# Kernel optimization log

Measured on AMD Instinct MI355X. Metric: run time of the kernel, lower is better.

## Reference

```python
import jax, jax.numpy as jnp
import numpy as np

NUM_EDGES = 4000
NODES_PER_EDGE = 25
D_IN = 128
NUM_PROJ = 128
NUM_ANCHORS = 64
EPS = 1e-5


def sparse_sort(src, index):
    """Per-column stable sort of src (N,P), grouped by 1D segment index (N,).
    Mirrors the repo's sparse_sort: min-max normalize to [0,1] then add segment id."""
    fmin = src.min(axis=0, keepdims=True)
    fmax = src.max(axis=0, keepdims=True)
    norm = (src - fmin) / (fmax - fmin + 1e-12) + index[:, None].astype(src.dtype)
    perm = jnp.argsort(norm, axis=0, stable=True)  # (N, P)
    return jnp.take_along_axis(src, perm, axis=0), perm


def setup_inputs() -> dict:
    key = jax.random.key(0)
    k1, k2, k3 = jax.random.split(key, 3)
    n_inc = NUM_EDGES * NODES_PER_EDGE
    X = jax.random.normal(k1, (n_inc, D_IN), dtype=jnp.float32)
    # sorted segment ids, every edge has >=2 members -> double_self_loops is a no-op
    hyperedge_index = jnp.repeat(jnp.arange(NUM_EDGES, dtype=jnp.int32), NODES_PER_EDGE)
    theta_v = jax.random.normal(k2, (NUM_PROJ, D_IN), dtype=jnp.float32)
    # reference anchors: linspace(-1,1,M) replicated over projections (as in __init__)
    ref_anchors = jnp.tile(jnp.linspace(-1.0, 1.0, NUM_ANCHORS, dtype=jnp.float32)[:, None], (1, NUM_PROJ))
    weight = jax.random.normal(k3, (NUM_PROJ, NUM_ANCHORS), dtype=jnp.float32) * 0.1
    return {"X": X, "theta_v": theta_v, "ref_anchors": ref_anchors, "weight": weight,
            "hyperedge_index": hyperedge_index, "num_edges": NUM_EDGES}


def reference(X, theta_v, ref_anchors, weight, hyperedge_index, num_edges):
    P = theta_v.shape[0]
    M = ref_anchors.shape[0]
    dt = X.dtype
    # weight_norm with g=1: rows of v normalized to unit L2
    W = theta_v / jnp.linalg.norm(theta_v, axis=1, keepdims=True)
    Xslices = X @ W.T  # (N, P) slices
    Xslices_sorted, perm = sparse_sort(Xslices, hyperedge_index)
    seg = hyperedge_index[perm[:, 0]]  # segment id per sorted row (N,)
    N = seg.shape[0]
    # per-segment degree, pointer offsets
    D1 = jax.ops.segment_sum(jnp.ones(N, dt), seg, num_segments=num_edges)  # (E,)
    ptr = jnp.concatenate([jnp.zeros(1, dt), jnp.cumsum(D1)])
    D = D1[seg]
    Pofs = ptr[seg]
    R = jnp.arange(N, dtype=dt) + 1.0
    # sample positions: within-segment quantile in (0,1) + segment offset -> globally sorted
    x = (R - Pofs - 1.0) / (D - 1.0) * 0.99999 + EPS + seg.astype(dt)  # (N,)
    edges = jnp.arange(num_edges, dtype=jnp.int32)
    grid = jnp.linspace(0.0, 1.0, M).astype(dt) * 0.99998 + EPS  # (M,)
    xnew = (edges[:, None].astype(dt) + grid[None, :]).reshape(-1)  # (E*M,)
    # interp1d: x/xnew identical across projections -> one searchsorted, broadcast interp
    y = Xslices_sorted.T  # (P, N)
    ind = jnp.clip(jnp.searchsorted(x, xnew), 1, N - 1)  # (E*M,)
    x0, x1 = x[ind - 1], x[ind]
    t = ((xnew - x0) / (x1 - x0))[None, :]  # (1, E*M)
    ynew = y[:, ind - 1] + (y[:, ind] - y[:, ind - 1]) * t  # (P, E*M)
    Xsi = ynew.T  # (E*M, P)
    # reference slices per edge, sorted within segments (identity for sorted anchors)
    seg_anchor = jnp.repeat(edges, M)  # (E*M,)
    Rslices = jnp.tile(ref_anchors, (num_edges, 1))  # (E*M, P)
    _, Rind = sparse_sort(Rslices, seg_anchor)
    emb = Rslices - jnp.take_along_axis(Xsi, Rind, axis=0)  # (E*M, P)
    emb = emb.T.reshape(P, num_edges, M)
    out = (weight[:, None, :] * emb).mean(-1).T  # (E, P)
    return out, edges
```

## Files before the change

kernel.cpp:

```cpp
#include <hip/hip_runtime.h>
#include <math.h>

#define NEDGE 4000
#define NPE   25
#define DIN   128
#define NPROJ 128
#define NANCH 64
#define NROWS (NEDGE*NPE)
#define NBLK  (NROWS/32)

__device__ __forceinline__ float xval_of(int g) {
  int ee = g / NPE;
  int jj = g - ee * NPE;
  float t1 = __fdiv_rn((float)jj, 24.0f);
  float t2 = __fmul_rn(t1, 0.99999f);
  float t3 = __fadd_rn(t2, 1e-5f);
  return __fadd_rn(t3, (float)ee);
}

__global__ __launch_bounds__(128) void k_prep(const float* __restrict__ theta,
                                              const float* __restrict__ anchors,
                                              const float* __restrict__ weight,
                                              float* __restrict__ Wt,
                                              float* __restrict__ awT) {
  int p = threadIdx.x;
  float s = 0.f;
  #pragma unroll 8
  for (int k = 0; k < DIN; ++k) { float t = theta[p*DIN + k]; s = fmaf(t, t, s); }
  float nrm = sqrtf(s);
  for (int k = 0; k < DIN; ++k)
    Wt[k*NPROJ + p] = __fdiv_rn(theta[p*DIN + k], nrm);
  #pragma unroll
  for (int m = 0; m < NANCH; ++m) {
    awT[(2*m    )*NPROJ + p] = anchors[m*NPROJ + p];
    awT[(2*m + 1)*NPROJ + p] = weight[p*NANCH + m];
  }
}

__global__ __launch_bounds__(256) void k_gemm(const float* __restrict__ X,
                                              const float* __restrict__ Wt,
                                              float* __restrict__ Xs,
                                              float* __restrict__ pmin,
                                              float* __restrict__ pmax) {
  __shared__ float sW[32 * NPROJ];
  __shared__ float sX[32 * DIN];
  const int tid = threadIdx.x;
  const int rbase = blockIdx.x * 32;
  {
    const float4* src = (const float4*)(X + (size_t)rbase * DIN);
    float4* dst = (float4*)sX;
    #pragma unroll
    for (int i = 0; i < 4; ++i) dst[tid + 256*i] = src[tid + 256*i];
  }
  const int cg = tid & 31, rg = tid >> 5;
  const int p0 = cg * 4, r0 = rg * 4;
  float acc[4][4] = {};
  for (int ph = 0; ph < 4; ++ph) {
    __syncthreads();
    {
      const float4* src = (const float4*)(Wt + ph * 32 * NPROJ);
      float4* dst = (float4*)sW;
      #pragma unroll
      for (int i = 0; i < 4; ++i) dst[tid + 256*i] = src[tid + 256*i];
    }
    __syncthreads();
    #pragma unroll
    for (int k0 = 0; k0 < 32; k0 += 4) {
      float4 w[4];
      #pragma unroll
      for (int i = 0; i < 4; ++i) w[i] = *(const float4*)&sW[(k0+i)*NPROJ + p0];
      #pragma unroll
      for (int i = 0; i < 4; ++i) {
        float4 xv = *(const float4*)&sX[(r0+i)*DIN + ph*32 + k0];
        const float xs[4] = {xv.x, xv.y, xv.z, xv.w};
        #pragma unroll
        for (int kk = 0; kk < 4; ++kk) {
          acc[i][0] = fmaf(xs[kk], w[kk].x, acc[i][0]);
          acc[i][1] = fmaf(xs[kk], w[kk].y, acc[i][1]);
          acc[i][2] = fmaf(xs[kk], w[kk].z, acc[i][2]);
          acc[i][3] = fmaf(xs[kk], w[kk].w, acc[i][3]);
        }
      }
    }
  }
  #pragma unroll
  for (int i = 0; i < 4; ++i) {
    float4 st = make_float4(acc[i][0], acc[i][1], acc[i][2], acc[i][3]);
    *(float4*)&Xs[(size_t)(rbase + r0 + i)*NPROJ + p0] = st;
  }
  __syncthreads();
  float* rmn = sX;
  float* rmx = sX + 8*NPROJ;
  #pragma unroll
  for (int c = 0; c < 4; ++c) {
    float mn = fminf(fminf(acc[0][c], acc[1][c]), fminf(acc[2][c], acc[3][c]));
    float mx = fmaxf(fmaxf(acc[0][c], acc[1][c]), fmaxf(acc[2][c], acc[3][c]));
    rmn[rg*NPROJ + p0 + c] = mn;
    rmx[rg*NPROJ + p0 + c] = mx;
  }
  __syncthreads();
  if (tid < NPROJ) {
    float mn = rmn[tid], mx = rmx[tid];
    #pragma unroll
    for (int g2 = 1; g2 < 8; ++g2) {
      mn = fminf(mn, rmn[g2*NPROJ + tid]);
      mx = fmaxf(mx, rmx[g2*NPROJ + tid]);
    }
    pmin[(size_t)blockIdx.x*NPROJ + tid] = mn;
    pmax[(size_t)blockIdx.x*NPROJ + tid] = mx;
  }
}

__global__ __launch_bounds__(256) void k_red1(const float* __restrict__ pmin,
                                              const float* __restrict__ pmax,
                                              float* __restrict__ imn,
                                              float* __restrict__ imx) {
  __shared__ float smn[NPROJ], smx[NPROJ];
  const int tid = threadIdx.x, p = tid & 127, h = tid >> 7;
  const int b = blockIdx.x;
  float mn = INFINITY, mx = -INFINITY;
  for (int s = 125*b + h; s < 125*(b+1); s += 2) {
    mn = fminf(mn, pmin[(size_t)s*NPROJ + p]);
    mx = fmaxf(mx, pmax[(size_t)s*NPROJ + p]);
  }
  if (h == 1) { smn[p] = mn; smx[p] = mx; }
  __syncthreads();
  if (h == 0) {
    imn[b*NPROJ + p] = fminf(mn, smn[p]);
    imx[b*NPROJ + p] = fmaxf(mx, smx[p]);
  }
}

__global__ __launch_bounds__(256) void k_red2(const float* __restrict__ imn,
                                              const float* __restrict__ imx,
                                              float* __restrict__ fmn,
                                              float* __restrict__ fmx) {
  __shared__ float smn[NPROJ], smx[NPROJ];
  const int tid = threadIdx.x, p = tid & 127, h = tid >> 7;
  float mn = INFINITY, mx = -INFINITY;
  for (int s = h; s < 25; s += 2) {
    mn = fminf(mn, imn[s*NPROJ + p]);
    mx = fmaxf(mx, imx[s*NPROJ + p]);
  }
  if (h == 1) { smn[p] = mn; smx[p] = mx; }
  __syncthreads();
  if (h == 0) { fmn[p] = fminf(mn, smn[p]); fmx[p] = fmaxf(mx, smx[p]); }
}

__global__ __launch_bounds__(128) void k_sort(float* Xs,
                                              const float* __restrict__ fmnA,
                                              const float* __restrict__ fmxA) {
  __shared__ float svals[NPE * NPROJ];
  const int e = blockIdx.x;
  const int p = threadIdx.x;
  const float ef = (float)e;
  const float fmin = fmnA[p];
  const float denom = __fadd_rn(__fsub_rn(fmxA[p], fmin), 1e-12f);

  float v[NPE];
  unsigned ku[NPE];
  #pragma unroll
  for (int j = 0; j < NPE; ++j) {
    float x = Xs[(size_t)(e*NPE + j)*NPROJ + p];
    v[j] = x;
    ku[j] = __float_as_uint(__fadd_rn(__fdiv_rn(__fsub_rn(x, fmin), denom), ef));
  }
  #pragma unroll
  for (int i = 0; i < NPE; ++i) {
    int cnt = 0;
    #pragma unroll
    for (int j = 0; j < NPE; ++j) {
      if (j == i) continue;
      cnt += (j < i) ? (ku[j] <= ku[i]) : (ku[j] < ku[i]);
    }
    svals[cnt*NPROJ + p] = v[i];
  }
  #pragma unroll
  for (int j = 0; j < NPE; ++j)
    Xs[(size_t)(e*NPE + j)*NPROJ + p] = svals[j*NPROJ + p];
}

__global__ __launch_bounds__(128) void k_epi(const float* __restrict__ Xs,
                                             const float* __restrict__ awT,
                                             float* __restrict__ out) {
  __shared__ float sv[(NPE + 2) * NPROJ];
  __shared__ int   sind[NANCH];
  __shared__ float stt[NANCH];
  const int e = blockIdx.x;
  const int p = threadIdx.x;
  const float ef = (float)e;

  if (e > 0) {
    sv[p]         = Xs[(size_t)((e-1)*NPE + 23)*NPROJ + p];
    sv[NPROJ + p] = Xs[(size_t)((e-1)*NPE + 24)*NPROJ + p];
  }
  #pragma unroll
  for (int j = 0; j < NPE; ++j)
    sv[(2 + j)*NPROJ + p] = Xs[(size_t)(e*NPE + j)*NPROJ + p];

  if (p < NANCH) {
    const int m = p;
    const float delta = __fdiv_rn(1.0f, 63.0f);
    float g = __fmul_rn((float)m, delta);
    g = __fadd_rn(__fmul_rn(g, 0.99998f), 1e-5f);
    const float xnew = __fadd_rn(ef, g);
    int lo = e*NPE - 1; if (lo < 0) lo = 0;
    const int hi = e*NPE + (NPE - 1);
    int ind = -1;
    for (int j = lo; j <= hi; ++j) {
      float xg = xval_of(j);
      if (ind < 0 && xg >= xnew) ind = j;
    }
    if (ind < 0) ind = hi;
    if (ind < 1) ind = 1;
    float x0 = xval_of(ind - 1);
    float x1 = xval_of(ind);
    stt[m]  = __fdiv_rn(__fsub_rn(xnew, x0), __fsub_rn(x1, x0));
    sind[m] = ind;
  }
  __syncthreads();

  float acc = 0.f;
  const int base = e * NPE;
  for (int m = 0; m < NANCH; ++m) {
    const int ind = sind[m];
    const float t = stt[m];
    const int o1 = ind - base;
    const float y1 = sv[(o1 + 2)*NPROJ + p];
    const float y0 = sv[(o1 + 1)*NPROJ + p];
    const float ynew = __fadd_rn(y0, __fmul_rn(__fsub_rn(y1, y0), t));
    const float emb  = __fsub_rn(awT[(2*m)*NPROJ + p], ynew);
    acc = __fadd_rn(acc, __fmul_rn(awT[(2*m + 1)*NPROJ + p], emb));
  }
  out[(size_t)e*NPROJ + p] = __fmul_rn(acc, 0.015625f);
  if (p == 0) out[NEDGE*NPROJ + e] = (float)e;
}

extern "C" void kernel_launch(void* const* d_in, const int* in_sizes, int n_in,
                              void* d_out, int out_size, void* d_ws, size_t ws_size,
                              hipStream_t stream) {
  (void)in_sizes; (void)n_in; (void)out_size; (void)ws_size;
  const float* X      = (const float*)d_in[0];
  const float* theta  = (const float*)d_in[1];
  const float* anchor = (const float*)d_in[2];
  const float* weight = (const float*)d_in[3];
  float* out = (float*)d_out;
  float* ws  = (float*)d_ws;

  float* Xs   = ws;
  float* Wt   = Xs   + (size_t)NROWS*NPROJ;
  float* awT  = Wt   + DIN*NPROJ;
  float* pmin = awT  + 2*NANCH*NPROJ;
  float* pmax = pmin + (size_t)NBLK*NPROJ;
  float* imn  = pmax + (size_t)NBLK*NPROJ;
  float* imx  = imn  + 25*NPROJ;
  float* fmn  = imx  + 25*NPROJ;
  float* fmx  = fmn  + NPROJ;

  k_prep<<<1, 128, 0, stream>>>(theta, anchor, weight, Wt, awT);
  k_gemm<<<NBLK, 256, 0, stream>>>(X, Wt, Xs, pmin, pmax);
  k_red1<<<25, 256, 0, stream>>>(pmin, pmax, imn, imx);
  k_red2<<<1, 256, 0, stream>>>(imn, imx, fmn, fmx);
  k_sort<<<NEDGE, 128, 0, stream>>>(Xs, fmn, fmx);
  k_epi <<<NEDGE, 128, 0, stream>>>(Xs, awT, out);
}
```

Before: 219.3 us.

## Fuse per-edge sort into epilogue kernel and parallelize prep kernel

The separate sort kernel, which wrote the sorted slices back to global memory, is merged into the epilogue kernel. Each edge now sorts its 25 rows straight into shared memory. The two boundary values needed from the previous edge are recomputed by scanning that edge's 25 rows for its two largest keys, so no global write-back or re-read is needed. The prep kernel also goes from one 128-thread block with serial loops to 192 blocks. The cost is that every block reads its predecessor edge's data again and adds a selection pass.

```diff
diff --git a/kernel.cpp b/kernel.cpp
--- a/kernel.cpp
+++ b/kernel.cpp
@@ -23,17 +23,23 @@
                                               const float* __restrict__ weight,
                                               float* __restrict__ Wt,
                                               float* __restrict__ awT) {
-  int p = threadIdx.x;
-  float s = 0.f;
-  #pragma unroll 8
-  for (int k = 0; k < DIN; ++k) { float t = theta[p*DIN + k]; s = fmaf(t, t, s); }
-  float nrm = sqrtf(s);
-  for (int k = 0; k < DIN; ++k)
-    Wt[k*NPROJ + p] = __fdiv_rn(theta[p*DIN + k], nrm);
-  #pragma unroll
-  for (int m = 0; m < NANCH; ++m) {
-    awT[(2*m    )*NPROJ + p] = anchors[m*NPROJ + p];
-    awT[(2*m + 1)*NPROJ + p] = weight[p*NANCH + m];
+  __shared__ float snrm;
+  const int t = threadIdx.x;
+  if (blockIdx.x < NPROJ) {
+    const int p = blockIdx.x;
+    if (t == 0) {
+      float s = 0.f;
+      #pragma unroll 8
+      for (int k = 0; k < DIN; ++k) { float x = theta[p*DIN + k]; s = fmaf(x, x, s); }
+      snrm = sqrtf(s);
+    }
+    __syncthreads();
+    const float nrm = snrm;
+    Wt[t*NPROJ + p] = __fdiv_rn(theta[p*DIN + t], nrm);
+  } else {
+    const int m = blockIdx.x - NPROJ;
+    awT[(2*m    )*NPROJ + t] = anchors[m*NPROJ + t];
+    awT[(2*m + 1)*NPROJ + t] = weight[t*NANCH + m];
   }
 }
 
@@ -147,56 +153,57 @@
   if (h == 0) { fmn[p] = fminf(mn, smn[p]); fmx[p] = fmaxf(mx, smx[p]); }
 }
 
-__global__ __launch_bounds__(128) void k_sort(float* Xs,
+__global__ __launch_bounds__(128) void k_main(const float* __restrict__ Xs,
                                               const float* __restrict__ fmnA,
-                                              const float* __restrict__ fmxA) {
-  __shared__ float svals[NPE * NPROJ];
-  const int e = blockIdx.x;
-  const int p = threadIdx.x;
-  const float ef = (float)e;
-  const float fmin = fmnA[p];
-  const float denom = __fadd_rn(__fsub_rn(fmxA[p], fmin), 1e-12f);
-
-  float v[NPE];
-  unsigned ku[NPE];
-  #pragma unroll
-  for (int j = 0; j < NPE; ++j) {
-    float x = Xs[(size_t)(e*NPE + j)*NPROJ + p];
-    v[j] = x;
-    ku[j] = __float_as_uint(__fadd_rn(__fdiv_rn(__fsub_rn(x, fmin), denom), ef));
-  }
-  #pragma unroll
-  for (int i = 0; i < NPE; ++i) {
-    int cnt = 0;
-    #pragma unroll
-    for (int j = 0; j < NPE; ++j) {
-      if (j == i) continue;
-      cnt += (j < i) ? (ku[j] <= ku[i]) : (ku[j] < ku[i]);
-    }
-    svals[cnt*NPROJ + p] = v[i];
-  }
-  #pragma unroll
-  for (int j = 0; j < NPE; ++j)
-    Xs[(size_t)(e*NPE + j)*NPROJ + p] = svals[j*NPROJ + p];
-}
-
-__global__ __launch_bounds__(128) void k_epi(const float* __restrict__ Xs,
-                                             const float* __restrict__ awT,
-                                             float* __restrict__ out) {
+                                              const float* __restrict__ fmxA,
+                                              const float* __restrict__ awT,
+                                              float* __restrict__ out) {
   __shared__ float sv[(NPE + 2) * NPROJ];
   __shared__ int   sind[NANCH];
   __shared__ float stt[NANCH];
   const int e = blockIdx.x;
   const int p = threadIdx.x;
   const float ef = (float)e;
-
+  const float fmin = fmnA[p];
+  const float denom = __fadd_rn(__fsub_rn(fmxA[p], fmin), 1e-12f);
+
+  float v[NPE], pv[NPE];
+  #pragma unroll
+  for (int j = 0; j < NPE; ++j) v[j] = Xs[(size_t)(e*NPE + j)*NPROJ + p];
   if (e > 0) {
-    sv[p]         = Xs[(size_t)((e-1)*NPE + 23)*NPROJ + p];
-    sv[NPROJ + p] = Xs[(size_t)((e-1)*NPE + 24)*NPROJ + p];
-  }
+    #pragma unroll
+    for (int j = 0; j < NPE; ++j) pv[j] = Xs[(size_t)((e-1)*NPE + j)*NPROJ + p];
+  }
+
+  unsigned ku[NPE];
   #pragma unroll
   for (int j = 0; j < NPE; ++j)
-    sv[(2 + j)*NPROJ + p] = Xs[(size_t)(e*NPE + j)*NPROJ + p];
+    ku[j] = __float_as_uint(__fadd_rn(__fdiv_rn(__fsub_rn(v[j], fmin), denom), ef));
+  #pragma unroll
+  for (int i = 0; i < NPE; ++i) {
+    int cnt = 0;
+    #pragma unroll
+    for (int j = 0; j < NPE; ++j) {
+      if (j == i) continue;
+      cnt += (j < i) ? (ku[j] <= ku[i]) : (ku[j] < ku[i]);
+    }
+    sv[(2 + cnt)*NPROJ + p] = v[i];
+  }
+
+  if (e > 0) {
+    const float efp = (float)(e - 1);
+    unsigned k1 = 0u, k2 = 0u;
+    float v1 = 0.f, v2 = 0.f;
+    #pragma unroll
+    for (int j = 0; j < NPE; ++j) {
+      unsigned kk = __float_as_uint(
+          __fadd_rn(__fdiv_rn(__fsub_rn(pv[j], fmin), denom), efp));
+      if (kk >= k1)      { k2 = k1; v2 = v1; k1 = kk; v1 = pv[j]; }
+      else if (kk >= k2) { k2 = kk; v2 = pv[j]; }
+    }
+    sv[p]         = v2;
+    sv[NPROJ + p] = v1;
+  }
 
   if (p < NANCH) {
     const int m = p;
@@ -257,10 +264,9 @@
   float* fmn  = imx  + 25*NPROJ;
   float* fmx  = fmn  + NPROJ;
 
-  k_prep<<<1, 128, 0, stream>>>(theta, anchor, weight, Wt, awT);
+  k_prep<<<NPROJ + NANCH, 128, 0, stream>>>(theta, anchor, weight, Wt, awT);
   k_gemm<<<NBLK, 256, 0, stream>>>(X, Wt, Xs, pmin, pmax);
   k_red1<<<25, 256, 0, stream>>>(pmin, pmax, imn, imx);
   k_red2<<<1, 256, 0, stream>>>(imn, imx, fmn, fmx);
-  k_sort<<<NEDGE, 128, 0, stream>>>(Xs, fmn, fmx);
-  k_epi <<<NEDGE, 128, 0, stream>>>(Xs, awT, out);
-}
+  k_main<<<NEDGE, 128, 0, stream>>>(Xs, fmn, fmx, awT, out);
+}
```

New measurement: 201.4 us. 8.2% less time.
